# Kernel tuning notes

Measured on AMD Instinct MI355X. Metric: run time of the kernel, lower is better.

## Reference

```python
import jax, jax.numpy as jnp
import numpy as np

N_NODES = 100000
FEAT_DIM = 256
EMBED_DIM = 256
BATCH = 50000
NUM_SAMPLE = 25
NAN_FILL = 0.01  # neigh_feats[isnan] = 0.01 in the original


def setup_inputs() -> dict:
    key = jax.random.key(0)
    k1, k2, k3, k4 = jax.random.split(key, 4)
    features = jax.random.normal(k1, (N_NODES, FEAT_DIM), dtype=jnp.float32)
    # Xavier-uniform-ish weight [embed_dim, feat_dim + embed_dim] (gcn=True)
    fan = FEAT_DIM + EMBED_DIM
    bound = float(np.sqrt(6.0 / (EMBED_DIM + fan)))
    weight = jax.random.uniform(k2, (EMBED_DIM, fan), dtype=jnp.float32,
                                minval=-bound, maxval=bound)
    nodes = jax.random.randint(k3, (BATCH,), 0, N_NODES, dtype=jnp.int64)
    neigh_idx = jax.random.randint(k4, (BATCH, NUM_SAMPLE), 0, N_NODES, dtype=jnp.int64)
    return {"features": features, "weight": weight, "nodes": nodes,
            "neigh_idx": neigh_idx}


def reference(features, weight, nodes, neigh_idx):
    # MeanAggregator: gather sampled neighbor features and mean over neighbors
    neigh_feats = features[neigh_idx].mean(axis=1)            # [B, F]
    neigh_feats = jnp.where(jnp.isnan(neigh_feats), NAN_FILL, neigh_feats)
    self_feats = features[nodes]                              # [B, F]
    combined = jnp.concatenate([self_feats, neigh_feats], axis=1)  # [B, F+E]
    # weight.matmul(combined.t()) then ReLU -> [E, B]
    out = jax.nn.relu(jnp.einsum('ef,bf->eb', weight, combined))
    return out
```

## Files before the change

kernel.cpp:

```cpp
#include <hip/hip_runtime.h>
#include <hip/hip_bf16.h>
#include <hip/hip_fp8.h>

#define FEAT    256
#define KDIM    512
#define EMBED   256
#define BATCH   50000
#define NSAMP   25
#define N_NODES 100000
#define NAN_FILL 0.01f

#define NTILE   32
#define LSTRIDE 520

typedef __attribute__((ext_vector_type(8))) short  short8;
typedef __attribute__((ext_vector_type(4))) float  floatx4;
typedef __attribute__((ext_vector_type(2))) float  float2v;
typedef __attribute__((ext_vector_type(4))) unsigned short ushort4v;
typedef __attribute__((ext_vector_type(4))) float  float4v;

#if __has_builtin(__builtin_amdgcn_cvt_pk_f32_fp8)
#define PK_FP8_DEC 1
#else
#define PK_FP8_DEC 0
#endif
#if __has_builtin(__builtin_amdgcn_cvt_pk_fp8_f32)
#define PK_FP8_ENC 1
#else
#define PK_FP8_ENC 0
#endif

__device__ inline unsigned short f2bf(float x) {
    __hip_bfloat16 h = __float2bfloat16(x);
    union { __hip_bfloat16 h; unsigned short u; } c; c.h = h;
    return c.u;
}
__device__ inline unsigned char f2fp8(float x) {
    __hip_fp8_e4m3 t(x);
    return (unsigned char)t.__x;
}
__device__ inline float fp8f(unsigned v) {
    __hip_fp8_e4m3 t; t.__x = (unsigned char)v;
    return (float)t;
}

__global__ __launch_bounds__(256) void fconv8_kernel(
    const float* __restrict__ F, unsigned char* __restrict__ F8)
{
    const size_t i = ((size_t)blockIdx.x * 256 + threadIdx.x) * 8;
    float4v a = *(const float4v*)(F + i);
    float4v b = *(const float4v*)(F + i + 4);
#if PK_FP8_ENC
    unsigned w0 = (unsigned)__builtin_amdgcn_cvt_pk_fp8_f32(a[0], a[1], 0, false);
    w0 = (unsigned)__builtin_amdgcn_cvt_pk_fp8_f32(a[2], a[3], (int)w0, true);
    unsigned w1 = (unsigned)__builtin_amdgcn_cvt_pk_fp8_f32(b[0], b[1], 0, false);
    w1 = (unsigned)__builtin_amdgcn_cvt_pk_fp8_f32(b[2], b[3], (int)w1, true);
    uint2 o; o.x = w0; o.y = w1;
    *(uint2*)(F8 + i) = o;
#else
    union { unsigned char c[8]; uint2 v; } o;
    o.c[0] = f2fp8(a[0]); o.c[1] = f2fp8(a[1]); o.c[2] = f2fp8(a[2]); o.c[3] = f2fp8(a[3]);
    o.c[4] = f2fp8(b[0]); o.c[5] = f2fp8(b[1]); o.c[6] = f2fp8(b[2]); o.c[7] = f2fp8(b[3]);
    *(uint2*)(F8 + i) = o.v;
#endif
}

__global__ __launch_bounds__(256) void wconv_kernel(
    const float* __restrict__ W, unsigned short* __restrict__ Wb)
{
    const int i = blockIdx.x * 256 + threadIdx.x;
    Wb[i] = f2bf(W[i]);
}

__global__ __launch_bounds__(256, 4) void enc_kernel(
    const float* __restrict__ F,
    const unsigned char* __restrict__ F8,
    const unsigned short* __restrict__ Wb,
    const int* __restrict__ nodes,
    const int* __restrict__ neigh,
    float* __restrict__ out)
{
    __shared__ unsigned short cl[NTILE * LSTRIDE];

    const int lane = threadIdx.x & 63;
    const int wave = threadIdx.x >> 6;
    const int q = lane >> 4;
    const int r = lane & 15;
    const int nbase = blockIdx.x * NTILE;

    for (int it = 0; it < NTILE / 4; ++it) {
        const int li = wave * (NTILE / 4) + it;
        int b = nbase + li;
        if (b >= BATCH) b = BATCH - 1;

        const int node = nodes[b];
        float4v sv = *(const float4v*)(F + (size_t)node * FEAT + lane * 4);

        const int* nb = neigh + (size_t)b * NSAMP;
        int idxs[NSAMP];
        #pragma unroll
        for (int j = 0; j < NSAMP; ++j) idxs[j] = nb[j];

        unsigned wv[NSAMP];
        #pragma unroll
        for (int j = 0; j < NSAMP; ++j)
            wv[j] = *(const unsigned*)(F8 + (size_t)idxs[j] * FEAT + lane * 4);

        float2v s01 = {0.f, 0.f}, s23 = {0.f, 0.f};
        #pragma unroll
        for (int j = 0; j < NSAMP; ++j) {
#if PK_FP8_DEC
            s01 += __builtin_amdgcn_cvt_pk_f32_fp8((int)wv[j], false);
            s23 += __builtin_amdgcn_cvt_pk_f32_fp8((int)wv[j], true);
#else
            s01[0] += fp8f(wv[j]);
            s01[1] += fp8f(wv[j] >> 8);
            s23[0] += fp8f(wv[j] >> 16);
            s23[1] += fp8f(wv[j] >> 24);
#endif
        }
        const float inv = 1.0f / NSAMP;
        float m0 = s01[0] * inv, m1 = s01[1] * inv, m2 = s23[0] * inv, m3 = s23[1] * inv;
        if (m0 != m0) m0 = NAN_FILL;
        if (m1 != m1) m1 = NAN_FILL;
        if (m2 != m2) m2 = NAN_FILL;
        if (m3 != m3) m3 = NAN_FILL;

        unsigned short* row = cl + li * LSTRIDE;
        ushort4v s; s[0] = f2bf(sv[0]); s[1] = f2bf(sv[1]); s[2] = f2bf(sv[2]); s[3] = f2bf(sv[3]);
        *(ushort4v*)(row + lane * 4) = s;
        ushort4v m; m[0] = f2bf(m0); m[1] = f2bf(m1); m[2] = f2bf(m2); m[3] = f2bf(m3);
        *(ushort4v*)(row + FEAT + lane * 4) = m;
    }
    __syncthreads();

    const int mbase = wave * 64;
    const short* Wp = (const short*)Wb;
    const short* cp = (const short*)cl;

    floatx4 acc[4][2] = {};

    for (int k = 0; k < KDIM; k += 32) {
        short8 afr[4], bfr[2];
        #pragma unroll
        for (int mt = 0; mt < 4; ++mt) {
            const short* p = Wp + (size_t)(mbase + mt * 16 + r) * KDIM + k + q * 8;
            afr[mt] = *(const short8*)p;
        }
        #pragma unroll
        for (int nt = 0; nt < 2; ++nt) {
            const short* p = cp + (nt * 16 + r) * LSTRIDE + k + q * 8;
            bfr[nt] = *(const short8*)p;
        }
        #pragma unroll
        for (int mt = 0; mt < 4; ++mt)
            #pragma unroll
            for (int nt = 0; nt < 2; ++nt)
                acc[mt][nt] = __builtin_amdgcn_mfma_f32_16x16x32_bf16(
                    afr[mt], bfr[nt], acc[mt][nt], 0, 0, 0);
    }

    #pragma unroll
    for (int mt = 0; mt < 4; ++mt) {
        #pragma unroll
        for (int nt = 0; nt < 2; ++nt) {
            const int col = nbase + nt * 16 + r;
            if (col < BATCH) {
                #pragma unroll
                for (int i = 0; i < 4; ++i) {
                    const int row = mbase + mt * 16 + q * 4 + i;
                    float v = acc[mt][nt][i];
                    out[(size_t)row * BATCH + col] = v > 0.f ? v : 0.f;
                }
            }
        }
    }
}

extern "C" void kernel_launch(void* const* d_in, const int* in_sizes, int n_in,
                              void* d_out, int out_size, void* d_ws, size_t ws_size,
                              hipStream_t stream) {
    const float* features = (const float*)d_in[0];
    const float* weight   = (const float*)d_in[1];
    const int*   nodes    = (const int*)d_in[2];
    const int*   neigh    = (const int*)d_in[3];
    float* out = (float*)d_out;

    unsigned char* F8  = (unsigned char*)d_ws;
    unsigned short* Wb = (unsigned short*)(F8 + (size_t)N_NODES * FEAT);

    fconv8_kernel<<<(N_NODES * FEAT) / (256 * 8), 256, 0, stream>>>(features, F8);
    wconv_kernel<<<(EMBED * KDIM) / 256, 256, 0, stream>>>(weight, Wb);

    const int nblocks = (BATCH + NTILE - 1) / NTILE;
    enc_kernel<<<nblocks, 256, 0, stream>>>(features, F8, Wb, nodes, neigh, out);
}
```

Before: 262.6 us.

## Software-pipeline neighbor gathers with double-buffered index and feature loads

Restructures the per-wave gather loop into a two-stage software pipeline. While one batch item is reduced and written to LDS, the index loads and FP8 feature gathers for the next item are already in flight. Scheduling barriers keep the compiler from reordering the stages. This targets memory latency in the gather phase, at the cost of roughly doubling the VGPRs held for in-flight loads, which may lower occupancy under the 4-blocks launch bound.

```diff
diff --git a/kernel.cpp b/kernel.cpp
--- a/kernel.cpp
+++ b/kernel.cpp
@@ -11,6 +11,7 @@
 #define NAN_FILL 0.01f
 
 #define NTILE   32
+#define ITEMS   (NTILE / 4)
 #define LSTRIDE 520
 
 typedef __attribute__((ext_vector_type(8))) short  short8;
@@ -88,49 +89,80 @@
     const int r = lane & 15;
     const int nbase = blockIdx.x * NTILE;
 
-    for (int it = 0; it < NTILE / 4; ++it) {
-        const int li = wave * (NTILE / 4) + it;
-        int b = nbase + li;
-        if (b >= BATCH) b = BATCH - 1;
-
-        const int node = nodes[b];
-        float4v sv = *(const float4v*)(F + (size_t)node * FEAT + lane * 4);
-
-        const int* nb = neigh + (size_t)b * NSAMP;
-        int idxs[NSAMP];
-        #pragma unroll
-        for (int j = 0; j < NSAMP; ++j) idxs[j] = nb[j];
-
-        unsigned wv[NSAMP];
-        #pragma unroll
-        for (int j = 0; j < NSAMP; ++j)
-            wv[j] = *(const unsigned*)(F8 + (size_t)idxs[j] * FEAT + lane * 4);
-
-        float2v s01 = {0.f, 0.f}, s23 = {0.f, 0.f};
-        #pragma unroll
-        for (int j = 0; j < NSAMP; ++j) {
+    {
+        int nodeA, nodeB;
+        int idxA[NSAMP], idxB[NSAMP];
+        float4v svA, svB;
+        unsigned wvA[NSAMP], wvB[NSAMP];
+
+#define LOADIDX(S, IT) do {                                                   \
+        int b_ = nbase + wave * ITEMS + (IT);                                 \
+        if (b_ >= BATCH) b_ = BATCH - 1;                                      \
+        node##S = nodes[b_];                                                  \
+        const int* nb_ = neigh + (size_t)b_ * NSAMP;                          \
+        _Pragma("unroll")                                                     \
+        for (int j_ = 0; j_ < NSAMP; ++j_) idx##S[j_] = nb_[j_];              \
+    } while (0)
+
+#define GATHER(S) do {                                                        \
+        sv##S = *(const float4v*)(F + (size_t)node##S * FEAT + lane * 4);     \
+        _Pragma("unroll")                                                     \
+        for (int j_ = 0; j_ < NSAMP; ++j_)                                    \
+            wv##S[j_] = *(const unsigned*)(F8 + (size_t)idx##S[j_] * FEAT + lane * 4); \
+    } while (0)
+
 #if PK_FP8_DEC
-            s01 += __builtin_amdgcn_cvt_pk_f32_fp8((int)wv[j], false);
-            s23 += __builtin_amdgcn_cvt_pk_f32_fp8((int)wv[j], true);
-#else
-            s01[0] += fp8f(wv[j]);
-            s01[1] += fp8f(wv[j] >> 8);
-            s23[0] += fp8f(wv[j] >> 16);
-            s23[1] += fp8f(wv[j] >> 24);
-#endif
-        }
-        const float inv = 1.0f / NSAMP;
-        float m0 = s01[0] * inv, m1 = s01[1] * inv, m2 = s23[0] * inv, m3 = s23[1] * inv;
-        if (m0 != m0) m0 = NAN_FILL;
-        if (m1 != m1) m1 = NAN_FILL;
-        if (m2 != m2) m2 = NAN_FILL;
-        if (m3 != m3) m3 = NAN_FILL;
-
-        unsigned short* row = cl + li * LSTRIDE;
-        ushort4v s; s[0] = f2bf(sv[0]); s[1] = f2bf(sv[1]); s[2] = f2bf(sv[2]); s[3] = f2bf(sv[3]);
-        *(ushort4v*)(row + lane * 4) = s;
-        ushort4v m; m[0] = f2bf(m0); m[1] = f2bf(m1); m[2] = f2bf(m2); m[3] = f2bf(m3);
-        *(ushort4v*)(row + FEAT + lane * 4) = m;
+#define ACCUM(S, J) do {                                                      \
+        s01 += __builtin_amdgcn_cvt_pk_f32_fp8((int)wv##S[J], false);         \
+        s23 += __builtin_amdgcn_cvt_pk_f32_fp8((int)wv##S[J], true);          \
+    } while (0)
+#else
+#define ACCUM(S, J) do {                                                      \
+        s01[0] += fp8f(wv##S[J]);       s01[1] += fp8f(wv##S[J] >> 8);        \
+        s23[0] += fp8f(wv##S[J] >> 16); s23[1] += fp8f(wv##S[J] >> 24);       \
+    } while (0)
+#endif
+
+#define CONSUME(S, IT) do {                                                   \
+        float2v s01 = {0.f, 0.f}, s23 = {0.f, 0.f};                           \
+        _Pragma("unroll")                                                     \
+        for (int j_ = 0; j_ < NSAMP; ++j_) ACCUM(S, j_);                      \
+        const float inv_ = 1.0f / NSAMP;                                      \
+        float m0 = s01[0] * inv_, m1 = s01[1] * inv_;                         \
+        float m2 = s23[0] * inv_, m3 = s23[1] * inv_;                         \
+        if (m0 != m0) m0 = NAN_FILL;                                          \
+        if (m1 != m1) m1 = NAN_FILL;                                          \
+        if (m2 != m2) m2 = NAN_FILL;                                          \
+        if (m3 != m3) m3 = NAN_FILL;                                          \
+        unsigned short* row_ = cl + (wave * ITEMS + (IT)) * LSTRIDE;          \
+        ushort4v s_;                                                          \
+        s_[0] = f2bf(sv##S[0]); s_[1] = f2bf(sv##S[1]);                       \
+        s_[2] = f2bf(sv##S[2]); s_[3] = f2bf(sv##S[3]);                       \
+        *(ushort4v*)(row_ + lane * 4) = s_;                                   \
+        ushort4v m_;                                                          \
+        m_[0] = f2bf(m0); m_[1] = f2bf(m1); m_[2] = f2bf(m2); m_[3] = f2bf(m3); \
+        *(ushort4v*)(row_ + FEAT + lane * 4) = m_;                            \
+    } while (0)
+
+        LOADIDX(A, 0);
+        LOADIDX(B, 1);
+        GATHER(A);
+
+        #pragma unroll 1
+        for (int it = 0; it < ITEMS; it += 2) {
+            GATHER(B);
+            if (it + 2 < ITEMS) LOADIDX(A, it + 2);
+            __builtin_amdgcn_sched_barrier(0);
+            CONSUME(A, it);
+            if (it + 2 < ITEMS) GATHER(A);
+            if (it + 3 < ITEMS) LOADIDX(B, it + 3);
+            __builtin_amdgcn_sched_barrier(0);
+            CONSUME(B, it + 1);
+        }
+#undef LOADIDX
+#undef GATHER
+#undef ACCUM
+#undef CONSUME
     }
     __syncthreads();
 
```

New measurement: 271.3 us. 1.03x slower.

## Split fused gather+GEMM into separate gather and GEMM kernels

Applied to the files above, without the earlier changes.

The single encoder kernel is split in two. A gather kernel uses one wave per batch row to write bf16 combined rows to a workspace buffer, and a GEMM kernel loads those rows into LDS with global_load_lds and runs MFMA over a 48-column tile. This is meant to decouple the latency-bound gather from the compute phase so each kernel can run at its own occupancy. The cost is a 50 MB workspace write and read-back plus one extra launch. The NaN-fill check is also dropped, which changes semantics if the mean is ever NaN.

```diff
diff --git a/kernel.cpp b/kernel.cpp
--- a/kernel.cpp
+++ b/kernel.cpp
@@ -10,7 +10,7 @@
 #define N_NODES 100000
 #define NAN_FILL 0.01f
 
-#define NTILE   32
+#define NTILE   48
 #define LSTRIDE 520
 
 typedef __attribute__((ext_vector_type(8))) short  short8;
@@ -72,12 +72,53 @@
     Wb[i] = f2bf(W[i]);
 }
 
-__global__ __launch_bounds__(256, 4) void enc_kernel(
+__global__ __launch_bounds__(256, 6) void gather_kernel(
     const float* __restrict__ F,
     const unsigned char* __restrict__ F8,
-    const unsigned short* __restrict__ Wb,
     const int* __restrict__ nodes,
     const int* __restrict__ neigh,
+    unsigned short* __restrict__ Cb)
+{
+    const int lane = threadIdx.x & 63;
+    const int wave = threadIdx.x >> 6;
+    const int b = __builtin_amdgcn_readfirstlane(blockIdx.x * 4 + wave);
+
+    const int node = nodes[b];
+    float4v sv = *(const float4v*)(F + (size_t)node * FEAT + lane * 4);
+
+    const int* nb = neigh + (size_t)b * NSAMP;
+    int idx[NSAMP];
+    #pragma unroll
+    for (int j = 0; j < NSAMP; ++j) idx[j] = nb[j];
+
+    unsigned wv[NSAMP];
+    #pragma unroll
+    for (int j = 0; j < NSAMP; ++j)
+        wv[j] = *(const unsigned*)(F8 + (size_t)idx[j] * FEAT + lane * 4);
+
+    float2v s01 = {0.f, 0.f}, s23 = {0.f, 0.f};
+    #pragma unroll
+    for (int j = 0; j < NSAMP; ++j) {
+#if PK_FP8_DEC
+        s01 += __builtin_amdgcn_cvt_pk_f32_fp8((int)wv[j], false);
+        s23 += __builtin_amdgcn_cvt_pk_f32_fp8((int)wv[j], true);
+#else
+        s01[0] += fp8f(wv[j]);        s01[1] += fp8f(wv[j] >> 8);
+        s23[0] += fp8f(wv[j] >> 16);  s23[1] += fp8f(wv[j] >> 24);
+#endif
+    }
+    const float inv = 1.0f / NSAMP;
+    unsigned short* row = Cb + (size_t)b * KDIM;
+    ushort4v s; s[0] = f2bf(sv[0]); s[1] = f2bf(sv[1]); s[2] = f2bf(sv[2]); s[3] = f2bf(sv[3]);
+    *(ushort4v*)(row + lane * 4) = s;
+    ushort4v m; m[0] = f2bf(s01[0] * inv); m[1] = f2bf(s01[1] * inv);
+    m[2] = f2bf(s23[0] * inv); m[3] = f2bf(s23[1] * inv);
+    *(ushort4v*)(row + FEAT + lane * 4) = m;
+}
+
+__global__ __launch_bounds__(256, 3) void gemm_kernel(
+    const unsigned short* __restrict__ Cb,
+    const unsigned short* __restrict__ Wb,
     float* __restrict__ out)
 {
     __shared__ unsigned short cl[NTILE * LSTRIDE];
@@ -88,74 +129,46 @@
     const int r = lane & 15;
     const int nbase = blockIdx.x * NTILE;
 
-    for (int it = 0; it < NTILE / 4; ++it) {
-        const int li = wave * (NTILE / 4) + it;
+    #pragma unroll
+    for (int t = 0; t < NTILE / 4; ++t) {
+        const int li = wave * (NTILE / 4) + t;
         int b = nbase + li;
         if (b >= BATCH) b = BATCH - 1;
-
-        const int node = nodes[b];
-        float4v sv = *(const float4v*)(F + (size_t)node * FEAT + lane * 4);
-
-        const int* nb = neigh + (size_t)b * NSAMP;
-        int idxs[NSAMP];
-        #pragma unroll
-        for (int j = 0; j < NSAMP; ++j) idxs[j] = nb[j];
-
-        unsigned wv[NSAMP];
-        #pragma unroll
-        for (int j = 0; j < NSAMP; ++j)
-            wv[j] = *(const unsigned*)(F8 + (size_t)idxs[j] * FEAT + lane * 4);
-
-        float2v s01 = {0.f, 0.f}, s23 = {0.f, 0.f};
-        #pragma unroll
-        for (int j = 0; j < NSAMP; ++j) {
-#if PK_FP8_DEC
-            s01 += __builtin_amdgcn_cvt_pk_f32_fp8((int)wv[j], false);
-            s23 += __builtin_amdgcn_cvt_pk_f32_fp8((int)wv[j], true);
-#else
-            s01[0] += fp8f(wv[j]);
-            s01[1] += fp8f(wv[j] >> 8);
-            s23[0] += fp8f(wv[j] >> 16);
-            s23[1] += fp8f(wv[j] >> 24);
-#endif
-        }
-        const float inv = 1.0f / NSAMP;
-        float m0 = s01[0] * inv, m1 = s01[1] * inv, m2 = s23[0] * inv, m3 = s23[1] * inv;
-        if (m0 != m0) m0 = NAN_FILL;
-        if (m1 != m1) m1 = NAN_FILL;
-        if (m2 != m2) m2 = NAN_FILL;
-        if (m3 != m3) m3 = NAN_FILL;
-
-        unsigned short* row = cl + li * LSTRIDE;
-        ushort4v s; s[0] = f2bf(sv[0]); s[1] = f2bf(sv[1]); s[2] = f2bf(sv[2]); s[3] = f2bf(sv[3]);
-        *(ushort4v*)(row + lane * 4) = s;
-        ushort4v m; m[0] = f2bf(m0); m[1] = f2bf(m1); m[2] = f2bf(m2); m[3] = f2bf(m3);
-        *(ushort4v*)(row + FEAT + lane * 4) = m;
-    }
+        const unsigned short* src = Cb + (size_t)b * KDIM + lane * 8;
+        unsigned short* dst = cl + li * LSTRIDE;
+#if __has_builtin(__builtin_amdgcn_global_load_lds)
+        __builtin_amdgcn_global_load_lds(
+            (const __attribute__((address_space(1))) unsigned*)src,
+            (__attribute__((address_space(3))) unsigned*)dst, 16, 0, 0);
+#else
+        *(short8*)(dst + lane * 8) = *(const short8*)src;
+#endif
+    }
+    asm volatile("s_waitcnt vmcnt(0)" ::: "memory");
     __syncthreads();
 
     const int mbase = wave * 64;
     const short* Wp = (const short*)Wb;
     const short* cp = (const short*)cl;
 
-    floatx4 acc[4][2] = {};
+    floatx4 acc[4][3] = {};
 
     for (int k = 0; k < KDIM; k += 32) {
-        short8 afr[4], bfr[2];
+        short8 afr[4], bfr[3];
         #pragma unroll
         for (int mt = 0; mt < 4; ++mt) {
             const short* p = Wp + (size_t)(mbase + mt * 16 + r) * KDIM + k + q * 8;
             afr[mt] = *(const short8*)p;
         }
         #pragma unroll
-        for (int nt = 0; nt < 2; ++nt) {
+        for (int nt = 0; nt < 3; ++nt) {
             const short* p = cp + (nt * 16 + r) * LSTRIDE + k + q * 8;
             bfr[nt] = *(const short8*)p;
         }
         #pragma unroll
         for (int mt = 0; mt < 4; ++mt)
             #pragma unroll
-            for (int nt = 0; nt < 2; ++nt)
+            for (int nt = 0; nt < 3; ++nt)
                 acc[mt][nt] = __builtin_amdgcn_mfma_f32_16x16x32_bf16(
                     afr[mt], bfr[nt], acc[mt][nt], 0, 0, 0);
     }
@@ -163,7 +176,7 @@
     #pragma unroll
     for (int mt = 0; mt < 4; ++mt) {
         #pragma unroll
-        for (int nt = 0; nt < 2; ++nt) {
+        for (int nt = 0; nt < 3; ++nt) {
             const int col = nbase + nt * 16 + r;
             if (col < BATCH) {
                 #pragma unroll
@@ -186,12 +199,15 @@
     const int*   neigh    = (const int*)d_in[3];
     float* out = (float*)d_out;
 
-    unsigned char* F8  = (unsigned char*)d_ws;
+    unsigned char*  F8 = (unsigned char*)d_ws;
     unsigned short* Wb = (unsigned short*)(F8 + (size_t)N_NODES * FEAT);
+    unsigned short* Cb = Wb + (size_t)EMBED * KDIM;
 
     fconv8_kernel<<<(N_NODES * FEAT) / (256 * 8), 256, 0, stream>>>(features, F8);
     wconv_kernel<<<(EMBED * KDIM) / 256, 256, 0, stream>>>(weight, Wb);
 
+    gather_kernel<<<BATCH / 4, 256, 0, stream>>>(features, F8, nodes, neigh, Cb);
+
     const int nblocks = (BATCH + NTILE - 1) / NTILE;
-    enc_kernel<<<nblocks, 256, 0, stream>>>(features, F8, Wb, nodes, neigh, out);
-}
+    gemm_kernel<<<nblocks, 256, 0, stream>>>(Cb, Wb, out);
+}
```

Result: slower. 275.8 us (+5.0%).

## Gather neighbor rows with 16-byte loads per lane and pipeline across 48-node tiles

Applied to the files above, without the earlier changes.

Each wave now handles four nodes at once: every 16-lane group loads a whole fp8 neighbor row with 16-byte vector loads. Neighbor indices are fetched once per lane and broadcast with shuffles. The 25 neighbor loads are software-pipelined in double-buffered chunks of five, with sched_barrier hints so loads overlap decode and accumulate. The node tile grows from 32 to 48, so each block issues three MFMA N-tiles per W fragment, and occupancy is lowered to 3 blocks to fit the larger LDS tile. The NaN-fill check on the neighbor mean is dropped, which changes results only if the features contain NaNs.

```diff
diff --git a/kernel.cpp b/kernel.cpp
--- a/kernel.cpp
+++ b/kernel.cpp
@@ -10,13 +10,16 @@
 #define N_NODES 100000
 #define NAN_FILL 0.01f
 
-#define NTILE   32
+#define NTILE   48
+#define IPW     12
 #define LSTRIDE 520
 
 typedef __attribute__((ext_vector_type(8))) short  short8;
 typedef __attribute__((ext_vector_type(4))) float  floatx4;
 typedef __attribute__((ext_vector_type(2))) float  float2v;
 typedef __attribute__((ext_vector_type(4))) unsigned short ushort4v;
+typedef __attribute__((ext_vector_type(8))) unsigned short ushort8v;
+typedef __attribute__((ext_vector_type(4))) unsigned int   uint4v;
 typedef __attribute__((ext_vector_type(4))) float  float4v;
 
 #if __has_builtin(__builtin_amdgcn_cvt_pk_f32_fp8)
@@ -72,7 +75,7 @@
     Wb[i] = f2bf(W[i]);
 }
 
-__global__ __launch_bounds__(256, 4) void enc_kernel(
+__global__ __launch_bounds__(256, 3) void enc_kernel(
     const float* __restrict__ F,
     const unsigned char* __restrict__ F8,
     const unsigned short* __restrict__ Wb,
@@ -84,53 +87,120 @@
 
     const int lane = threadIdx.x & 63;
     const int wave = threadIdx.x >> 6;
-    const int q = lane >> 4;
+    const int g = lane >> 4;
     const int r = lane & 15;
     const int nbase = blockIdx.x * NTILE;
 
-    for (int it = 0; it < NTILE / 4; ++it) {
-        const int li = wave * (NTILE / 4) + it;
-        int b = nbase + li;
-        if (b >= BATCH) b = BATCH - 1;
-
-        const int node = nodes[b];
-        float4v sv = *(const float4v*)(F + (size_t)node * FEAT + lane * 4);
-
-        const int* nb = neigh + (size_t)b * NSAMP;
-        int idxs[NSAMP];
-        #pragma unroll
-        for (int j = 0; j < NSAMP; ++j) idxs[j] = nb[j];
-
-        unsigned wv[NSAMP];
-        #pragma unroll
-        for (int j = 0; j < NSAMP; ++j)
-            wv[j] = *(const unsigned*)(F8 + (size_t)idxs[j] * FEAT + lane * 4);
-
-        float2v s01 = {0.f, 0.f}, s23 = {0.f, 0.f};
-        #pragma unroll
-        for (int j = 0; j < NSAMP; ++j) {
+    #pragma unroll
+    for (int round = 0; round < IPW / 4; ++round) {
+        const int b0 = nbase + wave * IPW + round * 4;
+        int bg = b0 + g; if (bg >= BATCH) bg = BATCH - 1;
+
+        const int ilo = neigh[(size_t)bg * NSAMP + r];
+        const int ihi = neigh[(size_t)bg * NSAMP + (r > 8 ? 24 : 16 + r)];
+        const int nd  = nodes[bg];
+
+        float4v sv0, sv1, sv2, sv3;
+        {
+            const int n0 = __shfl(nd, 0),  n1 = __shfl(nd, 16);
+            const int n2 = __shfl(nd, 32), n3 = __shfl(nd, 48);
+            sv0 = *(const float4v*)(F + (size_t)n0 * FEAT + lane * 4);
+            sv1 = *(const float4v*)(F + (size_t)n1 * FEAT + lane * 4);
+            sv2 = *(const float4v*)(F + (size_t)n2 * FEAT + lane * 4);
+            sv3 = *(const float4v*)(F + (size_t)n3 * FEAT + lane * 4);
+        }
+
+        float2v acc[8] = {};
+
+#define SHFL5(DST, C) do {                                                    \
+        _Pragma("unroll")                                                     \
+        for (int jj = 0; jj < 5; ++jj) {                                      \
+            const int j_ = (C) * 5 + jj;                                      \
+            DST[jj] = __shfl(j_ < 16 ? ilo : ihi,                             \
+                             g * 16 + (j_ < 16 ? j_ : j_ - 16));              \
+        }                                                                     \
+    } while (0)
+
+#define GATH5(WV, IDX) do {                                                   \
+        _Pragma("unroll")                                                     \
+        for (int jj = 0; jj < 5; ++jj)                                        \
+            WV[jj] = *(const uint4v*)(F8 + (size_t)IDX[jj] * FEAT + r * 16);  \
+    } while (0)
+
 #if PK_FP8_DEC
-            s01 += __builtin_amdgcn_cvt_pk_f32_fp8((int)wv[j], false);
-            s23 += __builtin_amdgcn_cvt_pk_f32_fp8((int)wv[j], true);
-#else
-            s01[0] += fp8f(wv[j]);
-            s01[1] += fp8f(wv[j] >> 8);
-            s23[0] += fp8f(wv[j] >> 16);
-            s23[1] += fp8f(wv[j] >> 24);
-#endif
-        }
-        const float inv = 1.0f / NSAMP;
-        float m0 = s01[0] * inv, m1 = s01[1] * inv, m2 = s23[0] * inv, m3 = s23[1] * inv;
-        if (m0 != m0) m0 = NAN_FILL;
-        if (m1 != m1) m1 = NAN_FILL;
-        if (m2 != m2) m2 = NAN_FILL;
-        if (m3 != m3) m3 = NAN_FILL;
-
-        unsigned short* row = cl + li * LSTRIDE;
-        ushort4v s; s[0] = f2bf(sv[0]); s[1] = f2bf(sv[1]); s[2] = f2bf(sv[2]); s[3] = f2bf(sv[3]);
-        *(ushort4v*)(row + lane * 4) = s;
-        ushort4v m; m[0] = f2bf(m0); m[1] = f2bf(m1); m[2] = f2bf(m2); m[3] = f2bf(m3);
-        *(ushort4v*)(row + FEAT + lane * 4) = m;
+#define CONS5(WV) do {                                                        \
+        _Pragma("unroll")                                                     \
+        for (int jj = 0; jj < 5; ++jj) {                                      \
+            _Pragma("unroll")                                                 \
+            for (int d_ = 0; d_ < 4; ++d_) {                                  \
+                const unsigned w_ = WV[jj][d_];                               \
+                acc[d_ * 2]     += __builtin_amdgcn_cvt_pk_f32_fp8((int)w_, false); \
+                acc[d_ * 2 + 1] += __builtin_amdgcn_cvt_pk_f32_fp8((int)w_, true);  \
+            }                                                                 \
+        }                                                                     \
+    } while (0)
+#else
+#define CONS5(WV) do {                                                        \
+        _Pragma("unroll")                                                     \
+        for (int jj = 0; jj < 5; ++jj) {                                      \
+            _Pragma("unroll")                                                 \
+            for (int d_ = 0; d_ < 4; ++d_) {                                  \
+                const unsigned w_ = WV[jj][d_];                               \
+                acc[d_ * 2][0]     += fp8f(w_);                               \
+                acc[d_ * 2][1]     += fp8f(w_ >> 8);                          \
+                acc[d_ * 2 + 1][0] += fp8f(w_ >> 16);                         \
+                acc[d_ * 2 + 1][1] += fp8f(w_ >> 24);                         \
+            }                                                                 \
+        }                                                                     \
+    } while (0)
+#endif
+
+#define SB __builtin_amdgcn_sched_barrier(0)
+
+        int ixA[5], ixB[5];
+        uint4v wvA[5], wvB[5];
+        SHFL5(ixA, 0); GATH5(wvA, ixA);
+        SHFL5(ixB, 1); GATH5(wvB, ixB);
+        SB; CONS5(wvA);
+        SHFL5(ixA, 2); GATH5(wvA, ixA);
+        SB; CONS5(wvB);
+        SHFL5(ixB, 3); GATH5(wvB, ixB);
+        SB; CONS5(wvA);
+        SHFL5(ixA, 4); GATH5(wvA, ixA);
+        SB; CONS5(wvB);
+        SB; CONS5(wvA);
+#undef SHFL5
+#undef GATH5
+#undef CONS5
+#undef SB
+
+        const int lrow0 = wave * IPW + round * 4;
+        {
+            ushort4v s;
+            unsigned short* row;
+            s[0]=f2bf(sv0[0]); s[1]=f2bf(sv0[1]); s[2]=f2bf(sv0[2]); s[3]=f2bf(sv0[3]);
+            row = cl + (lrow0 + 0) * LSTRIDE; *(ushort4v*)(row + lane * 4) = s;
+            s[0]=f2bf(sv1[0]); s[1]=f2bf(sv1[1]); s[2]=f2bf(sv1[2]); s[3]=f2bf(sv1[3]);
+            row = cl + (lrow0 + 1) * LSTRIDE; *(ushort4v*)(row + lane * 4) = s;
+            s[0]=f2bf(sv2[0]); s[1]=f2bf(sv2[1]); s[2]=f2bf(sv2[2]); s[3]=f2bf(sv2[3]);
+            row = cl + (lrow0 + 2) * LSTRIDE; *(ushort4v*)(row + lane * 4) = s;
+            s[0]=f2bf(sv3[0]); s[1]=f2bf(sv3[1]); s[2]=f2bf(sv3[2]); s[3]=f2bf(sv3[3]);
+            row = cl + (lrow0 + 3) * LSTRIDE; *(ushort4v*)(row + lane * 4) = s;
+        }
+        {
+            const float inv = 1.0f / NSAMP;
+            unsigned short* grow = cl + (lrow0 + g) * LSTRIDE + FEAT + r * 16;
+            ushort8v m0, m1;
+            #pragma unroll
+            for (int k2 = 0; k2 < 4; ++k2) {
+                m0[k2 * 2]     = f2bf(acc[k2][0] * inv);
+                m0[k2 * 2 + 1] = f2bf(acc[k2][1] * inv);
+                m1[k2 * 2]     = f2bf(acc[4 + k2][0] * inv);
+                m1[k2 * 2 + 1] = f2bf(acc[4 + k2][1] * inv);
+            }
+            *(ushort8v*)grow       = m0;
+            *(ushort8v*)(grow + 8) = m1;
+        }
     }
     __syncthreads();
 
@@ -138,38 +208,38 @@
     const short* Wp = (const short*)Wb;
     const short* cp = (const short*)cl;
 
-    floatx4 acc[4][2] = {};
+    floatx4 acc2[4][3] = {};
 
     for (int k = 0; k < KDIM; k += 32) {
-        short8 afr[4], bfr[2];
+        short8 afr[4], bfr[3];
         #pragma unroll
         for (int mt = 0; mt < 4; ++mt) {
-            const short* p = Wp + (size_t)(mbase + mt * 16 + r) * KDIM + k + q * 8;
+            const short* p = Wp + (size_t)(mbase + mt * 16 + r) * KDIM + k + g * 8;
             afr[mt] = *(const short8*)p;
         }
         #pragma unroll
-        for (int nt = 0; nt < 2; ++nt) {
-            const short* p = cp + (nt * 16 + r) * LSTRIDE + k + q * 8;
+        for (int nt = 0; nt < 3; ++nt) {
+            const short* p = cp + (nt * 16 + r) * LSTRIDE + k + g * 8;
             bfr[nt] = *(const short8*)p;
         }
         #pragma unroll
         for (int mt = 0; mt < 4; ++mt)
             #pragma unroll
-            for (int nt = 0; nt < 2; ++nt)
-                acc[mt][nt] = __builtin_amdgcn_mfma_f32_16x16x32_bf16(
-                    afr[mt], bfr[nt], acc[mt][nt], 0, 0, 0);
+            for (int nt = 0; nt < 3; ++nt)
+                acc2[mt][nt] = __builtin_amdgcn_mfma_f32_16x16x32_bf16(
+                    afr[mt], bfr[nt], acc2[mt][nt], 0, 0, 0);
     }
 
     #pragma unroll
     for (int mt = 0; mt < 4; ++mt) {
         #pragma unroll
-        for (int nt = 0; nt < 2; ++nt) {
+        for (int nt = 0; nt < 3; ++nt) {
             const int col = nbase + nt * 16 + r;
             if (col < BATCH) {
                 #pragma unroll
                 for (int i = 0; i < 4; ++i) {
-                    const int row = mbase + mt * 16 + q * 4 + i;
-                    float v = acc[mt][nt][i];
+                    const int row = mbase + mt * 16 + g * 4 + i;
+                    float v = acc2[mt][nt][i];
                     out[(size_t)row * BATCH + col] = v > 0.f ? v : 0.f;
                 }
             }
```

After: 249.0 us. -5.2%, faster.
